# Optimization experiments

Measured on AMD Instinct MI355X. Metric: run time of the kernel, lower is better.

The kernel has to match this reference:

```python
import jax, jax.numpy as jnp
import numpy as np

EPS = 1e-6

def setup_inputs() -> dict:
    key = jax.random.key(0)
    k1, k2, k3 = jax.random.split(key, 3)
    D = 1024
    return {
        "x": jax.random.normal(k1, (2, 2048, D), dtype=jnp.float32),
        "w_norm": jnp.ones((D,), dtype=jnp.float32),
        "w_qkv": jax.random.normal(k2, (3 * D, D), dtype=jnp.float32) * (1.0 / np.sqrt(D)),
        "w_out": jax.random.normal(k3, (D, D), dtype=jnp.float32) * (1.0 / np.sqrt(D)),
        "window_size": 128,
        "n_heads": 16,
    }

def reference(x, w_norm, w_qkv, w_out, window_size, n_heads):
    B, L, D = x.shape
    H = n_heads
    dh = D // H
    skip = x
    # RMSNorm
    rms = jnp.sqrt(jnp.mean(x * x, axis=-1, keepdims=True) + EPS)
    xn = w_norm * (x / rms)
    # QKV projection (torch Linear: y = x @ W.T)
    qkv = xn @ w_qkv.T  # [B, L, 3D]
    q, k, v = jnp.split(qkv, 3, axis=-1)
    q = q.reshape(B, L, H, dh).transpose(0, 2, 1, 3)  # [B,H,L,dh]
    k = k.reshape(B, L, H, dh).transpose(0, 2, 1, 3)
    v = v.reshape(B, L, H, dh).transpose(0, 2, 1, 3)
    scores = jnp.einsum("bhid,bhjd->bhij", q, k) / np.sqrt(dh)  # [B,H,L,L]
    # Symmetric window: token i attends to j in [i - w//2, i + w//2]
    idx = jnp.arange(L)
    half = window_size // 2
    band = jnp.abs(idx[:, None] - idx[None, :]) <= half  # [L, L]
    scores = jnp.where(band, scores, -jnp.inf)
    attn = jax.nn.softmax(scores, axis=-1)  # zeros outside band, matches torch loop
    out = jnp.einsum("bhij,bhjd->bhid", attn, v)  # [B,H,L,dh]
    out = out.transpose(0, 2, 1, 3).reshape(B, L, D)
    out = out @ w_out.T
    return out + skip
```

## Files before the change

### kernel.cpp

```cpp
#include <hip/hip_runtime.h>
#include <hip/hip_bf16.h>
#include <cstdint>

typedef float f32x4 __attribute__((ext_vector_type(4)));
typedef float f32x16 __attribute__((ext_vector_type(16)));
typedef short s16x8 __attribute__((ext_vector_type(8)));
typedef short s16x4 __attribute__((ext_vector_type(4)));
typedef unsigned int u32x2 __attribute__((ext_vector_type(2)));
typedef unsigned int u32x4 __attribute__((ext_vector_type(4)));

constexpr int B_ = 2, L_ = 2048, D_ = 1024, H_ = 16, DH = 64, HALF = 64;
constexpr int M_ROWS = B_ * L_;
constexpr int QKV_N = 3 * D_;

__device__ __forceinline__ void gload16(const void* g, void* l) {
    __builtin_amdgcn_global_load_lds(
        (const __attribute__((address_space(1))) unsigned int*)g,
        (__attribute__((address_space(3))) unsigned int*)l, 16, 0, 0);
}

__device__ __forceinline__ void cfence() {
    __builtin_amdgcn_sched_barrier(0);
    asm volatile("" ::: "memory");
}

__global__ __launch_bounds__(256) void prep_kernel(const float* __restrict__ x,
                                                   const float* __restrict__ wn,
                                                   const float* __restrict__ wq,
                                                   const float* __restrict__ wo,
                                                   __hip_bfloat16* __restrict__ xn,
                                                   __hip_bfloat16* __restrict__ oq,
                                                   __hip_bfloat16* __restrict__ oo) {
    constexpr int NQ4 = QKV_N * D_ / 4;
    constexpr int NCVT = NQ4 + D_ * D_ / 4;
    constexpr int CVTBLK = NCVT / 256;
    int bid = blockIdx.x;
    if (bid < CVTBLK) {
        int i = bid * 256 + threadIdx.x;
        const float* src; __hip_bfloat16* dst; int j;
        if (i < NQ4) { src = wq; dst = oq; j = i; }
        else         { src = wo; dst = oo; j = i - NQ4; }
        float4 v = reinterpret_cast<const float4*>(src)[j];
        s16x4 pk;
        float vals[4] = {v.x, v.y, v.z, v.w};
#pragma unroll
        for (int e = 0; e < 4; ++e) {
            __hip_bfloat16 t = __float2bfloat16(vals[e]);
            pk[e] = *reinterpret_cast<short*>(&t);
        }
        *(s16x4*)(dst + (size_t)j * 4) = pk;
    } else {
        int w = threadIdx.x >> 6, lane = threadIdx.x & 63;
        int row = (bid - CVTBLK) * 4 + w;
        const float4* xr = reinterpret_cast<const float4*>(x + (size_t)row * D_);
        const float4* wr = reinterpret_cast<const float4*>(wn);
        float4 v[4];
        float ss = 0.f;
#pragma unroll
        for (int c = 0; c < 4; ++c) {
            v[c] = xr[c * 64 + lane];
            ss += v[c].x * v[c].x + v[c].y * v[c].y + v[c].z * v[c].z + v[c].w * v[c].w;
        }
#pragma unroll
        for (int off = 32; off; off >>= 1) ss += __shfl_xor(ss, off);
        float rinv = rsqrtf(ss * (1.0f / D_) + 1e-6f);
#pragma unroll
        for (int c = 0; c < 4; ++c) {
            float4 wv = wr[c * 64 + lane];
            s16x4 pk;
            float vals[4] = {v[c].x * rinv * wv.x, v[c].y * rinv * wv.y,
                             v[c].z * rinv * wv.z, v[c].w * rinv * wv.w};
#pragma unroll
            for (int e = 0; e < 4; ++e) {
                __hip_bfloat16 t = __float2bfloat16(vals[e]);
                pk[e] = *reinterpret_cast<short*>(&t);
            }
            *(s16x4*)(xn + (size_t)row * D_ + (c * 64 + lane) * 4) = pk;
        }
    }
}

template <int EPI, int BN>
__global__ __launch_bounds__(256, 2) void gemm_pipe_kernel(const __hip_bfloat16* __restrict__ A,
                                                           const __hip_bfloat16* __restrict__ Bt,
                                                           __hip_bfloat16* __restrict__ Cbf,
                                                           __hip_bfloat16* __restrict__ vT,
                                                           float* __restrict__ Cf,
                                                           const float* __restrict__ resid,
                                                           int M, int N, int K) {
    constexpr int BM = 128;
    constexpr int NFR = BN / 32;
    constexpr int ABYTES = BM * 128;
    constexpr int BBYTES = BN * 128;
    constexpr int BUF = ABYTES + BBYTES;
    constexpr int AISS = BM / 32, BISS = BN / 32, NISS = AISS + BISS;
    __shared__ __align__(16) char smem[2 * BUF];

    const int tid = threadIdx.x;
    const int lane = tid & 63;
    const int wid = tid >> 6;

    int nwg = gridDim.x * gridDim.y;
    int lin = blockIdx.y * gridDim.x + blockIdx.x;
    int cpx = nwg >> 3;
    int swz = (lin & 7) * cpx + (lin >> 3);
    int bx = swz % gridDim.x;
    int by = swz / gridDim.x;

    const int rowBase = by * BM;
    const int colBase = bx * BN;
    const int NTILES = K >> 6;

    const int srow = tid >> 3;
    const int colSw = ((tid & 7) ^ (srow & 7)) << 3;
    const __hip_bfloat16* aG = A + (size_t)(rowBase + srow) * K + colSw;
    const __hip_bfloat16* bG = Bt + (size_t)(colBase + srow) * K + colSw;
    const int dstW = wid << 10;

    const int wm = wid >> 1, wn = wid & 1;
    const int l15 = lane & 15, hi = lane >> 4;
    const int s7 = l15 & 7;
    const int rA = wm * 64 + l15;
    const int rB = wn * (BN / 2) + l15;

    f32x4 acc[4][NFR];
#pragma unroll
    for (int m = 0; m < 4; ++m)
#pragma unroll
        for (int n = 0; n < NFR; ++n) acc[m][n] = (f32x4){0.f, 0.f, 0.f, 0.f};

#pragma unroll
    for (int i = 0; i < AISS; ++i) gload16(aG + (size_t)(i * 32) * K, smem + i * 4096 + dstW);
#pragma unroll
    for (int i = 0; i < BISS; ++i) gload16(bG + (size_t)(i * 32) * K, smem + ABYTES + i * 4096 + dstW);

    for (int kt = 0; kt < NTILES; ++kt) {
        const int bf = kt & 1;
        if (kt + 1 < NTILES) {
            char* base = smem + (bf ^ 1) * BUF;
            const __hip_bfloat16* as = aG + (size_t)(kt + 1) * 64;
            const __hip_bfloat16* bs = bG + (size_t)(kt + 1) * 64;
#pragma unroll
            for (int i = 0; i < AISS; ++i) gload16(as + (size_t)(i * 32) * K, base + i * 4096 + dstW);
#pragma unroll
            for (int i = 0; i < BISS; ++i) gload16(bs + (size_t)(i * 32) * K, base + ABYTES + i * 4096 + dstW);
            if constexpr (NISS == 8)
                asm volatile("s_waitcnt vmcnt(8)" ::: "memory");
            else
                asm volatile("s_waitcnt vmcnt(6)" ::: "memory");
        } else {
            asm volatile("s_waitcnt vmcnt(0)" ::: "memory");
        }
        __builtin_amdgcn_s_barrier();
        cfence();

        const char* ab = smem + bf * BUF;
        const char* bb = ab + ABYTES;
        s16x8 af[4][2], bfr[NFR][2];
#pragma unroll
        for (int mf = 0; mf < 4; ++mf)
#pragma unroll
            for (int kk = 0; kk < 2; ++kk)
                af[mf][kk] = *(const s16x8*)(ab + (rA + mf * 16) * 128 + (((kk * 4 + hi) ^ s7) << 4));
#pragma unroll
        for (int nf = 0; nf < NFR; ++nf)
#pragma unroll
            for (int kk = 0; kk < 2; ++kk)
                bfr[nf][kk] = *(const s16x8*)(bb + (rB + nf * 16) * 128 + (((kk * 4 + hi) ^ s7) << 4));

        __builtin_amdgcn_s_setprio(1);
#pragma unroll
        for (int kk = 0; kk < 2; ++kk)
#pragma unroll
            for (int mf = 0; mf < 4; ++mf)
#pragma unroll
                for (int nf = 0; nf < NFR; ++nf)
                    acc[mf][nf] = __builtin_amdgcn_mfma_f32_16x16x32_bf16(af[mf][kk], bfr[nf][kk],
                                                                          acc[mf][nf], 0, 0, 0);
        __builtin_amdgcn_s_setprio(0);

        asm volatile("s_waitcnt lgkmcnt(0)" ::: "memory");
        __builtin_amdgcn_s_barrier();
        cfence();
    }

    if constexpr (EPI == 0) {
        if (colBase < 2 * D_) {
#pragma unroll
            for (int mf = 0; mf < 4; ++mf)
#pragma unroll
                for (int nf = 0; nf < NFR; ++nf) {
                    int col = colBase + wn * (BN / 2) + nf * 16 + l15;
                    int row0 = rowBase + wm * 64 + mf * 16 + 4 * hi;
#pragma unroll
                    for (int r = 0; r < 4; ++r)
                        Cbf[(size_t)(row0 + r) * N + col] = __float2bfloat16(acc[mf][nf][r]);
                }
        } else {
            char* Ct = smem;
#pragma unroll
            for (int mf = 0; mf < 4; ++mf)
#pragma unroll
                for (int nf = 0; nf < NFR; ++nf) {
                    int cl = wn * (BN / 2) + nf * 16 + l15;
#pragma unroll
                    for (int r = 0; r < 4; ++r) {
                        int rl = wm * 64 + mf * 16 + 4 * hi + r;
                        __hip_bfloat16 t = __float2bfloat16(acc[mf][nf][r]);
                        *(short*)(Ct + cl * 272 + rl * 2) = *reinterpret_cast<short*>(&t);
                    }
                }
            __syncthreads();
            int cl = tid >> 1, half = tid & 1;
            int gcol = colBase + cl - 2 * D_;
            int hh = gcol >> 6, dd = gcol & 63;
            int bb2 = rowBase >> 11, i0 = rowBase & (L_ - 1);
            __hip_bfloat16* dstp = vT + ((size_t)(bb2 * H_ + hh) * DH + dd) * L_ + i0 + half * 64;
#pragma unroll
            for (int ch = 0; ch < 8; ++ch) {
                s16x8 vv = *(const s16x8*)(Ct + cl * 272 + half * 128 + ch * 16);
                *(s16x8*)(dstp + ch * 8) = vv;
            }
        }
    } else {
#pragma unroll
        for (int mf = 0; mf < 4; ++mf)
#pragma unroll
            for (int nf = 0; nf < NFR; ++nf) {
                int col = colBase + wn * (BN / 2) + nf * 16 + l15;
                int row0 = rowBase + wm * 64 + mf * 16 + 4 * hi;
#pragma unroll
                for (int r = 0; r < 4; ++r)
                    Cf[(size_t)(row0 + r) * N + col] = acc[mf][nf][r] + resid[(size_t)(row0 + r) * N + col];
            }
    }
}

__global__ __launch_bounds__(128, 2) void attn_mfma_kernel(const __hip_bfloat16* __restrict__ qkv,
                                                           const __hip_bfloat16* __restrict__ vT,
                                                           __hip_bfloat16* __restrict__ attn) {
    int tid = threadIdx.x;
    int w = tid >> 6;
    int lane = tid & 63;
    int l31 = lane & 31, hi1 = lane >> 5;
    int tq = blockIdx.x, h = blockIdx.y, b = blockIdx.z;
    int qbase = tq * 64 + 32 * w;
    int kb = qbase - HALF;
    int qg = qbase + l31;
    const __hip_bfloat16* qkvb = qkv + (size_t)(b * L_) * QKV_N;
    const __hip_bfloat16* vTg = vT + (size_t)(b * H_ + h) * DH * L_;

    s16x8 qf[4];
#pragma unroll
    for (int kk = 0; kk < 4; ++kk)
        qf[kk] = *(const s16x8*)(qkvb + (size_t)qg * QKV_N + h * DH + kk * 16 + hi1 * 8);

    f32x16 T[5];
#pragma unroll
    for (int kt = 0; kt < 5; ++kt) T[kt] = (f32x16)(0.f);
#pragma unroll
    for (int kt = 0; kt < 5; ++kt) {
        int keyg = kb + 32 * kt + l31;
        int kc = keyg < 0 ? 0 : (keyg > L_ - 1 ? L_ - 1 : keyg);
        const __hip_bfloat16* kp = qkvb + (size_t)kc * QKV_N + D_ + h * DH + hi1 * 8;
#pragma unroll
        for (int kk = 0; kk < 4; ++kk) {
            s16x8 kf = *(const s16x8*)(kp + kk * 16);
            T[kt] = __builtin_amdgcn_mfma_f32_32x32x16_bf16(kf, qf[kk], T[kt], 0, 0, 0);
        }
    }

    float mx = -1e30f;
#pragma unroll
    for (int kt = 0; kt < 5; ++kt) {
#pragma unroll
        for (int r = 0; r < 16; ++r) {
            int koff = (r & 3) + 8 * (r >> 2) + 4 * hi1;
            int keyg = kb + 32 * kt + koff;
            int del = keyg - qg;
            bool ok = (del >= -HALF) && (del <= HALF) && (keyg >= 0) && (keyg < L_);
            float t = ok ? T[kt][r] * 0.125f : -1e30f;
            T[kt][r] = t;
            mx = fmaxf(mx, t);
        }
    }
    mx = fmaxf(mx, __shfl_xor(mx, 32));
    float sum = 0.f;
#pragma unroll
    for (int kt = 0; kt < 5; ++kt) {
#pragma unroll
        for (int r = 0; r < 16; ++r) {
            float p = __expf(T[kt][r] - mx);
            T[kt][r] = p;
            sum += p;
        }
    }
    sum += __shfl_xor(sum, 32);
    float inv = 1.0f / sum;

    u32x4 pu[10];
#pragma unroll
    for (int kt = 0; kt < 5; ++kt) {
#pragma unroll
        for (int s = 0; s < 2; ++s) {
            unsigned P0, P1, P2, P3;
            asm("v_cvt_pk_bf16_f32 %0, %1, %2" : "=v"(P0) : "v"(T[kt][8 * s + 0]), "v"(T[kt][8 * s + 1]));
            asm("v_cvt_pk_bf16_f32 %0, %1, %2" : "=v"(P1) : "v"(T[kt][8 * s + 2]), "v"(T[kt][8 * s + 3]));
            asm("v_cvt_pk_bf16_f32 %0, %1, %2" : "=v"(P2) : "v"(T[kt][8 * s + 4]), "v"(T[kt][8 * s + 5]));
            asm("v_cvt_pk_bf16_f32 %0, %1, %2" : "=v"(P3) : "v"(T[kt][8 * s + 6]), "v"(T[kt][8 * s + 7]));
            u32x2 sA = __builtin_amdgcn_permlane32_swap(P0, P2, false, false);
            u32x2 sB = __builtin_amdgcn_permlane32_swap(P1, P3, false, false);
            pu[2 * kt + s] = (u32x4){sA[0], sB[0], sA[1], sB[1]};
        }
    }

    f32x16 O[2];
#pragma unroll
    for (int dt = 0; dt < 2; ++dt) O[dt] = (f32x16)(0.f);
#pragma unroll
    for (int t = 0; t < 10; ++t) {
        int kv = kb + 16 * t + 8 * hi1;
        kv = kv < 0 ? 0 : (kv > L_ - 8 ? L_ - 8 : kv);
        s16x8 pf = __builtin_bit_cast(s16x8, pu[t]);
#pragma unroll
        for (int dt = 0; dt < 2; ++dt) {
            s16x8 vf = *(const s16x8*)(vTg + (size_t)(32 * dt + l31) * L_ + kv);
            O[dt] = __builtin_amdgcn_mfma_f32_32x32x16_bf16(vf, pf, O[dt], 0, 0, 0);
        }
    }

    __hip_bfloat16* ob = attn + (size_t)(b * L_ + qg) * D_ + h * DH;
#pragma unroll
    for (int dt = 0; dt < 2; ++dt) {
#pragma unroll
        for (int rr = 0; rr < 4; ++rr) {
            s16x4 pk4;
#pragma unroll
            for (int j = 0; j < 4; ++j) {
                __hip_bfloat16 tb = __float2bfloat16(O[dt][4 * rr + j] * inv);
                pk4[j] = *reinterpret_cast<short*>(&tb);
            }
            *(s16x4*)(ob + 32 * dt + 8 * rr + 4 * hi1) = pk4;
        }
    }
}

extern "C" void kernel_launch(void* const* d_in, const int* in_sizes, int n_in,
                              void* d_out, int out_size, void* d_ws, size_t ws_size,
                              hipStream_t stream) {
    const float* x      = (const float*)d_in[0];
    const float* w_norm = (const float*)d_in[1];
    const float* w_qkv  = (const float*)d_in[2];
    const float* w_out  = (const float*)d_in[3];

    char* ws = (char*)d_ws;
    __hip_bfloat16* xn   = (__hip_bfloat16*)(ws);
    __hip_bfloat16* wq   = (__hip_bfloat16*)(ws + (8u  << 20));
    __hip_bfloat16* wo   = (__hip_bfloat16*)(ws + (14u << 20));
    __hip_bfloat16* qkv  = (__hip_bfloat16*)(ws + (16u << 20));
    __hip_bfloat16* attn = (__hip_bfloat16*)(ws + (40u << 20));
    __hip_bfloat16* vT   = (__hip_bfloat16*)(ws + (48u << 20));
    float* out = (float*)d_out;

    prep_kernel<<<4096 + M_ROWS / 4, 256, 0, stream>>>(x, w_norm, w_qkv, w_out, xn, wq, wo);

    gemm_pipe_kernel<0, 128><<<dim3(QKV_N / 128, M_ROWS / 128), 256, 0, stream>>>(
        xn, wq, qkv, vT, nullptr, nullptr, M_ROWS, QKV_N, D_);

    attn_mfma_kernel<<<dim3(L_ / 64, H_, B_), 128, 0, stream>>>(qkv, vT, attn);

    gemm_pipe_kernel<1, 64><<<dim3(D_ / 64, M_ROWS / 128), 256, 0, stream>>>(
        attn, wo, nullptr, nullptr, out, x, M_ROWS, D_, D_);
}
```

Measured before the change: 86.25 us.

## Switch GEMM to four-stage LDS ring with 32-wide K tiles

Replaces the double-buffered 64-wide K-tile loop with a four-slot ring of 32-wide K tiles, prefetching two tiles ahead. It uses a new swizzled LDS layout for loads and reads, and drops one barrier per iteration. The output GEMM gets a higher minimum-waves launch bound. The goal is to hide global-load latency better, at the cost of more loop iterations with fewer MFMAs each and possible register pressure under the tighter launch bound.

```diff
diff --git a/kernel.cpp b/kernel.cpp
--- a/kernel.cpp
+++ b/kernel.cpp
@@ -80,21 +80,21 @@
     }
 }
 
-template <int EPI, int BN>
-__global__ __launch_bounds__(256, 2) void gemm_pipe_kernel(const __hip_bfloat16* __restrict__ A,
-                                                           const __hip_bfloat16* __restrict__ Bt,
-                                                           __hip_bfloat16* __restrict__ Cbf,
-                                                           __hip_bfloat16* __restrict__ vT,
-                                                           float* __restrict__ Cf,
-                                                           const float* __restrict__ resid,
-                                                           int M, int N, int K) {
+template <int EPI, int BN, int MINW>
+__global__ __launch_bounds__(256, MINW) void gemm_pipe_kernel(const __hip_bfloat16* __restrict__ A,
+                                                              const __hip_bfloat16* __restrict__ Bt,
+                                                              __hip_bfloat16* __restrict__ Cbf,
+                                                              __hip_bfloat16* __restrict__ vT,
+                                                              float* __restrict__ Cf,
+                                                              const float* __restrict__ resid,
+                                                              int M, int N, int K) {
     constexpr int BM = 128;
     constexpr int NFR = BN / 32;
-    constexpr int ABYTES = BM * 128;
-    constexpr int BBYTES = BN * 128;
-    constexpr int BUF = ABYTES + BBYTES;
-    constexpr int AISS = BM / 32, BISS = BN / 32, NISS = AISS + BISS;
-    __shared__ __align__(16) char smem[2 * BUF];
+    constexpr int ATILE = BM * 64;
+    constexpr int BTILE = BN * 64;
+    constexpr int BUFB = ATILE + BTILE;
+    constexpr int AISS = BM / 64, BISS = BN / 64;
+    __shared__ __align__(16) char smem[4 * BUFB];
 
     const int tid = threadIdx.x;
     const int lane = tid & 63;
@@ -109,19 +109,20 @@
 
     const int rowBase = by * BM;
     const int colBase = bx * BN;
-    const int NTILES = K >> 6;
-
-    const int srow = tid >> 3;
-    const int colSw = ((tid & 7) ^ (srow & 7)) << 3;
-    const __hip_bfloat16* aG = A + (size_t)(rowBase + srow) * K + colSw;
-    const __hip_bfloat16* bG = Bt + (size_t)(colBase + srow) * K + colSw;
+    const int NTILES = K >> 5;
+
+    const int u = (tid & 7) ^ ((tid >> 3) & 7);
+    const int sRow = 2 * (tid >> 3) + (u >> 2);
+    const int sCol = (u & 3) * 8;
+    const __hip_bfloat16* aG = A + (size_t)(rowBase + sRow) * K + sCol;
+    const __hip_bfloat16* bG = Bt + (size_t)(colBase + sRow) * K + sCol;
     const int dstW = wid << 10;
 
     const int wm = wid >> 1, wn = wid & 1;
     const int l15 = lane & 15, hi = lane >> 4;
-    const int s7 = l15 & 7;
-    const int rA = wm * 64 + l15;
-    const int rB = wn * (BN / 2) + l15;
+    const int sRd = (((l15 & 1) << 2) | hi) ^ ((l15 >> 1) & 7);
+    const int aRd = wm * 4096 + (l15 >> 1) * 128 + sRd * 16;
+    const int bRd = ATILE + wn * (BN * 32) + (l15 >> 1) * 128 + sRd * 16;
 
     f32x4 acc[4][NFR];
 #pragma unroll
@@ -129,59 +130,57 @@
 #pragma unroll
         for (int n = 0; n < NFR; ++n) acc[m][n] = (f32x4){0.f, 0.f, 0.f, 0.f};
 
-#pragma unroll
-    for (int i = 0; i < AISS; ++i) gload16(aG + (size_t)(i * 32) * K, smem + i * 4096 + dstW);
-#pragma unroll
-    for (int i = 0; i < BISS; ++i) gload16(bG + (size_t)(i * 32) * K, smem + ABYTES + i * 4096 + dstW);
-
-    for (int kt = 0; kt < NTILES; ++kt) {
-        const int bf = kt & 1;
-        if (kt + 1 < NTILES) {
-            char* base = smem + (bf ^ 1) * BUF;
-            const __hip_bfloat16* as = aG + (size_t)(kt + 1) * 64;
-            const __hip_bfloat16* bs = bG + (size_t)(kt + 1) * 64;
-#pragma unroll
-            for (int i = 0; i < AISS; ++i) gload16(as + (size_t)(i * 32) * K, base + i * 4096 + dstW);
-#pragma unroll
-            for (int i = 0; i < BISS; ++i) gload16(bs + (size_t)(i * 32) * K, base + ABYTES + i * 4096 + dstW);
-            if constexpr (NISS == 8)
+    auto STAGE = [&](int tt) {
+        char* base = smem + ((tt & 3) * BUFB) + dstW;
+        const __hip_bfloat16* as = aG + (size_t)tt * 32;
+        const __hip_bfloat16* bs = bG + (size_t)tt * 32;
+#pragma unroll
+        for (int j = 0; j < AISS; ++j)
+            gload16(as + (size_t)(j * 64) * K, base + j * 4096);
+#pragma unroll
+        for (int j = 0; j < BISS; ++j)
+            gload16(bs + (size_t)(j * 64) * K, base + ATILE + j * 4096);
+    };
+
+    STAGE(0);
+    STAGE(1);
+
+    for (int t = 0; t < NTILES; ++t) {
+        if (t + 2 < NTILES) {
+            STAGE(t + 2);
+            if constexpr (AISS + BISS == 4)
                 asm volatile("s_waitcnt vmcnt(8)" ::: "memory");
             else
                 asm volatile("s_waitcnt vmcnt(6)" ::: "memory");
+        } else if (t + 1 < NTILES) {
+            if constexpr (AISS + BISS == 4)
+                asm volatile("s_waitcnt vmcnt(4)" ::: "memory");
+            else
+                asm volatile("s_waitcnt vmcnt(3)" ::: "memory");
         } else {
             asm volatile("s_waitcnt vmcnt(0)" ::: "memory");
         }
-        __builtin_amdgcn_s_barrier();
-        cfence();
-
-        const char* ab = smem + bf * BUF;
-        const char* bb = ab + ABYTES;
-        s16x8 af[4][2], bfr[NFR][2];
-#pragma unroll
-        for (int mf = 0; mf < 4; ++mf)
-#pragma unroll
-            for (int kk = 0; kk < 2; ++kk)
-                af[mf][kk] = *(const s16x8*)(ab + (rA + mf * 16) * 128 + (((kk * 4 + hi) ^ s7) << 4));
-#pragma unroll
-        for (int nf = 0; nf < NFR; ++nf)
-#pragma unroll
-            for (int kk = 0; kk < 2; ++kk)
-                bfr[nf][kk] = *(const s16x8*)(bb + (rB + nf * 16) * 128 + (((kk * 4 + hi) ^ s7) << 4));
-
-        __builtin_amdgcn_s_setprio(1);
-#pragma unroll
-        for (int kk = 0; kk < 2; ++kk)
-#pragma unroll
-            for (int mf = 0; mf < 4; ++mf)
-#pragma unroll
-                for (int nf = 0; nf < NFR; ++nf)
-                    acc[mf][nf] = __builtin_amdgcn_mfma_f32_16x16x32_bf16(af[mf][kk], bfr[nf][kk],
-                                                                          acc[mf][nf], 0, 0, 0);
-        __builtin_amdgcn_s_setprio(0);
-
         asm volatile("s_waitcnt lgkmcnt(0)" ::: "memory");
         __builtin_amdgcn_s_barrier();
         cfence();
+
+        const char* tb = smem + ((t & 3) * BUFB);
+        s16x8 af[4], bf[NFR];
+#pragma unroll
+        for (int mf = 0; mf < 4; ++mf)
+            af[mf] = *(const s16x8*)(tb + aRd + mf * 1024);
+#pragma unroll
+        for (int nf = 0; nf < NFR; ++nf)
+            bf[nf] = *(const s16x8*)(tb + bRd + nf * 1024);
+
+        __builtin_amdgcn_s_setprio(1);
+#pragma unroll
+        for (int mf = 0; mf < 4; ++mf)
+#pragma unroll
+            for (int nf = 0; nf < NFR; ++nf)
+                acc[mf][nf] = __builtin_amdgcn_mfma_f32_16x16x32_bf16(af[mf], bf[nf],
+                                                                      acc[mf][nf], 0, 0, 0);
+        __builtin_amdgcn_s_setprio(0);
     }
 
     if constexpr (EPI == 0) {
@@ -364,11 +363,11 @@
 
     prep_kernel<<<4096 + M_ROWS / 4, 256, 0, stream>>>(x, w_norm, w_qkv, w_out, xn, wq, wo);
 
-    gemm_pipe_kernel<0, 128><<<dim3(QKV_N / 128, M_ROWS / 128), 256, 0, stream>>>(
+    gemm_pipe_kernel<0, 128, 2><<<dim3(QKV_N / 128, M_ROWS / 128), 256, 0, stream>>>(
         xn, wq, qkv, vT, nullptr, nullptr, M_ROWS, QKV_N, D_);
 
     attn_mfma_kernel<<<dim3(L_ / 64, H_, B_), 128, 0, stream>>>(qkv, vT, attn);
 
-    gemm_pipe_kernel<1, 64><<<dim3(D_ / 64, M_ROWS / 128), 256, 0, stream>>>(
+    gemm_pipe_kernel<1, 64, 3><<<dim3(D_ / 64, M_ROWS / 128), 256, 0, stream>>>(
         attn, wo, nullptr, nullptr, out, x, M_ROWS, D_, D_);
 }
```

Result: slower. 88.90 us (+3.1%).

## Specialize QKV GEMM with 32-wide K tiles, higher occupancy, vectorized weight conversion

Applied to the files above, without the earlier changes.

Splits the templated GEMM into two dedicated kernels. The QKV GEMM now stages K in 32-wide tiles with a new swizzled LDS layout, halving shared memory so three blocks can be resident per CU, and does a two-pass vectorized V-transpose epilogue. The prep kernel converts 16 floats per thread instead of 4, writing 16-byte stores. The cost is twice as many K iterations with a barrier each, and the smaller tiles may raise sync overhead.

```diff
diff --git a/kernel.cpp b/kernel.cpp
--- a/kernel.cpp
+++ b/kernel.cpp
@@ -31,26 +31,38 @@
                                                    __hip_bfloat16* __restrict__ xn,
                                                    __hip_bfloat16* __restrict__ oq,
                                                    __hip_bfloat16* __restrict__ oo) {
-    constexpr int NQ4 = QKV_N * D_ / 4;
-    constexpr int NCVT = NQ4 + D_ * D_ / 4;
-    constexpr int CVTBLK = NCVT / 256;
+    constexpr int NQ16 = QKV_N * D_ / 16;
+    constexpr int NCVT16 = NQ16 + D_ * D_ / 16;
+    constexpr int CVTBLK = NCVT16 / 256;
     int bid = blockIdx.x;
+    int tid = threadIdx.x;
     if (bid < CVTBLK) {
-        int i = bid * 256 + threadIdx.x;
+        int i = bid * 256 + tid;
         const float* src; __hip_bfloat16* dst; int j;
-        if (i < NQ4) { src = wq; dst = oq; j = i; }
-        else         { src = wo; dst = oo; j = i - NQ4; }
-        float4 v = reinterpret_cast<const float4*>(src)[j];
-        s16x4 pk;
-        float vals[4] = {v.x, v.y, v.z, v.w};
-#pragma unroll
-        for (int e = 0; e < 4; ++e) {
-            __hip_bfloat16 t = __float2bfloat16(vals[e]);
-            pk[e] = *reinterpret_cast<short*>(&t);
-        }
-        *(s16x4*)(dst + (size_t)j * 4) = pk;
+        if (i < NQ16) { src = wq; dst = oq; j = i; }
+        else          { src = wo; dst = oo; j = i - NQ16; }
+        const float4* s4 = reinterpret_cast<const float4*>(src) + (size_t)j * 4;
+        float4 v[4];
+#pragma unroll
+        for (int c = 0; c < 4; ++c) v[c] = s4[c];
+        s16x8 p0, p1;
+#pragma unroll
+        for (int c = 0; c < 2; ++c) {
+            float vals[8] = {v[2*c].x, v[2*c].y, v[2*c].z, v[2*c].w,
+                             v[2*c+1].x, v[2*c+1].y, v[2*c+1].z, v[2*c+1].w};
+            s16x8 pk;
+#pragma unroll
+            for (int e = 0; e < 8; ++e) {
+                __hip_bfloat16 t = __float2bfloat16(vals[e]);
+                pk[e] = *reinterpret_cast<short*>(&t);
+            }
+            if (c == 0) p0 = pk; else p1 = pk;
+        }
+        __hip_bfloat16* o = dst + (size_t)j * 16;
+        *(s16x8*)(o) = p0;
+        *(s16x8*)(o + 8) = p1;
     } else {
-        int w = threadIdx.x >> 6, lane = threadIdx.x & 63;
+        int w = tid >> 6, lane = tid & 63;
         int row = (bid - CVTBLK) * 4 + w;
         const float4* xr = reinterpret_cast<const float4*>(x + (size_t)row * D_);
         const float4* wr = reinterpret_cast<const float4*>(wn);
@@ -80,21 +92,15 @@
     }
 }
 
-template <int EPI, int BN>
-__global__ __launch_bounds__(256, 2) void gemm_pipe_kernel(const __hip_bfloat16* __restrict__ A,
-                                                           const __hip_bfloat16* __restrict__ Bt,
-                                                           __hip_bfloat16* __restrict__ Cbf,
-                                                           __hip_bfloat16* __restrict__ vT,
-                                                           float* __restrict__ Cf,
-                                                           const float* __restrict__ resid,
-                                                           int M, int N, int K) {
-    constexpr int BM = 128;
-    constexpr int NFR = BN / 32;
-    constexpr int ABYTES = BM * 128;
-    constexpr int BBYTES = BN * 128;
-    constexpr int BUF = ABYTES + BBYTES;
-    constexpr int AISS = BM / 32, BISS = BN / 32, NISS = AISS + BISS;
-    __shared__ __align__(16) char smem[2 * BUF];
+__global__ __launch_bounds__(256, 3) void gemm_qkv_kernel(const __hip_bfloat16* __restrict__ A,
+                                                          const __hip_bfloat16* __restrict__ Bt,
+                                                          __hip_bfloat16* __restrict__ Cbf,
+                                                          __hip_bfloat16* __restrict__ vT,
+                                                          int M, int N, int K) {
+    constexpr int BOFF = 8192;
+    constexpr int BUFB = 16384;
+    constexpr int NT = 32;
+    __shared__ __align__(16) char smem[2 * BUFB];
 
     const int tid = threadIdx.x;
     const int lane = tid & 63;
@@ -107,6 +113,146 @@
     int bx = swz % gridDim.x;
     int by = swz / gridDim.x;
 
+    const int rowBase = by * 128;
+    const int colBase = bx * 128;
+
+    const int sR = tid >> 3;
+    const int su = (tid & 7) ^ (sR & 7);
+    const int sMrow = 2 * sR + (su >> 2);
+    const int sCol = (su & 3) * 8;
+    const __hip_bfloat16* aG0 = A + (size_t)(rowBase + sMrow) * K + sCol;
+    const __hip_bfloat16* aG1 = aG0 + (size_t)64 * K;
+    const __hip_bfloat16* bG0 = Bt + (size_t)(colBase + sMrow) * K + sCol;
+    const __hip_bfloat16* bG1 = bG0 + (size_t)64 * K;
+    const int dstW = wid << 10;
+
+    const int wm = wid >> 1, wn = wid & 1;
+    const int l15 = lane & 15, hi = lane >> 4;
+    const int sRd = (((l15 & 1) << 2) | hi) ^ ((l15 >> 1) & 7);
+    const int aRd = wm * 4096 + (l15 >> 1) * 128 + sRd * 16;
+    const int bRd = BOFF + wn * 4096 + (l15 >> 1) * 128 + sRd * 16;
+
+    f32x4 acc[4][4];
+#pragma unroll
+    for (int m = 0; m < 4; ++m)
+#pragma unroll
+        for (int n = 0; n < 4; ++n) acc[m][n] = (f32x4){0.f, 0.f, 0.f, 0.f};
+
+    auto STG = [&](int tt) {
+        char* base = smem + (tt & 1) * BUFB;
+        gload16(aG0 + (size_t)tt * 32, base + dstW);
+        gload16(aG1 + (size_t)tt * 32, base + 4096 + dstW);
+        gload16(bG0 + (size_t)tt * 32, base + BOFF + dstW);
+        gload16(bG1 + (size_t)tt * 32, base + BOFF + 4096 + dstW);
+    };
+
+    STG(0);
+
+    for (int t = 0; t < NT; ++t) {
+        if (t + 1 < NT) {
+            STG(t + 1);
+            asm volatile("s_waitcnt vmcnt(4)" ::: "memory");
+        } else {
+            asm volatile("s_waitcnt vmcnt(0)" ::: "memory");
+        }
+        __builtin_amdgcn_s_barrier();
+        cfence();
+
+        const char* tb = smem + (t & 1) * BUFB;
+        s16x8 af[4], bf[4];
+#pragma unroll
+        for (int mf = 0; mf < 4; ++mf)
+            af[mf] = *(const s16x8*)(tb + aRd + mf * 1024);
+#pragma unroll
+        for (int nf = 0; nf < 4; ++nf)
+            bf[nf] = *(const s16x8*)(tb + bRd + nf * 1024);
+
+        __builtin_amdgcn_s_setprio(1);
+#pragma unroll
+        for (int mf = 0; mf < 4; ++mf)
+#pragma unroll
+            for (int nf = 0; nf < 4; ++nf)
+                acc[mf][nf] = __builtin_amdgcn_mfma_f32_16x16x32_bf16(af[mf], bf[nf],
+                                                                      acc[mf][nf], 0, 0, 0);
+        __builtin_amdgcn_s_setprio(0);
+
+        asm volatile("s_waitcnt lgkmcnt(0)" ::: "memory");
+        __builtin_amdgcn_s_barrier();
+        cfence();
+    }
+
+    if (colBase < 2 * D_) {
+#pragma unroll
+        for (int mf = 0; mf < 4; ++mf)
+#pragma unroll
+            for (int nf = 0; nf < 4; ++nf) {
+                int col = colBase + wn * 64 + nf * 16 + l15;
+                int row0 = rowBase + wm * 64 + mf * 16 + 4 * hi;
+#pragma unroll
+                for (int r = 0; r < 4; ++r)
+                    Cbf[(size_t)(row0 + r) * N + col] = __float2bfloat16(acc[mf][nf][r]);
+            }
+    } else {
+        __syncthreads();
+        int bb2 = rowBase >> 11, i0 = rowBase & (L_ - 1);
+        char* Ct = smem;
+#pragma unroll
+        for (int p = 0; p < 2; ++p) {
+            if (p) __syncthreads();
+            if (wn == p) {
+#pragma unroll
+                for (int mf = 0; mf < 4; ++mf)
+#pragma unroll
+                    for (int nf = 0; nf < 4; ++nf) {
+                        int cl = nf * 16 + l15;
+                        int rlb = wm * 64 + mf * 16 + 4 * hi;
+                        s16x4 pk;
+#pragma unroll
+                        for (int r = 0; r < 4; ++r) {
+                            __hip_bfloat16 t = __float2bfloat16(acc[mf][nf][r]);
+                            pk[r] = *reinterpret_cast<short*>(&t);
+                        }
+                        *(s16x4*)(Ct + cl * 272 + rlb * 2) = pk;
+                    }
+            }
+            __syncthreads();
+            {
+                int c = tid >> 2, qd = tid & 3;
+                int gcol = colBase + p * 64 + c - 2 * D_;
+                int hh = gcol >> 6, dd = gcol & 63;
+                __hip_bfloat16* dstp = vT + ((size_t)(bb2 * H_ + hh) * DH + dd) * L_ + i0;
+#pragma unroll
+                for (int ch = 0; ch < 4; ++ch) {
+                    int rr = qd * 32 + ch * 8;
+                    *(s16x8*)(dstp + rr) = *(const s16x8*)(Ct + c * 272 + rr * 2);
+                }
+            }
+        }
+    }
+}
+
+__global__ __launch_bounds__(256, 2) void gemm_proj_kernel(const __hip_bfloat16* __restrict__ A,
+                                                           const __hip_bfloat16* __restrict__ Bt,
+                                                           float* __restrict__ Cf,
+                                                           const float* __restrict__ resid,
+                                                           int M, int N, int K) {
+    constexpr int BM = 128, BN = 64;
+    constexpr int ABYTES = BM * 128;
+    constexpr int BBYTES = BN * 128;
+    constexpr int BUF = ABYTES + BBYTES;
+    __shared__ __align__(16) char smem[2 * BUF];
+
+    const int tid = threadIdx.x;
+    const int lane = tid & 63;
+    const int wid = tid >> 6;
+
+    int nwg = gridDim.x * gridDim.y;
+    int lin = blockIdx.y * gridDim.x + blockIdx.x;
+    int cpx = nwg >> 3;
+    int swz = (lin & 7) * cpx + (lin >> 3);
+    int bx = swz % gridDim.x;
+    int by = swz / gridDim.x;
+
     const int rowBase = by * BM;
     const int colBase = bx * BN;
     const int NTILES = K >> 6;
@@ -121,49 +267,46 @@
     const int l15 = lane & 15, hi = lane >> 4;
     const int s7 = l15 & 7;
     const int rA = wm * 64 + l15;
-    const int rB = wn * (BN / 2) + l15;
-
-    f32x4 acc[4][NFR];
+    const int rB = wn * 32 + l15;
+
+    f32x4 acc[4][2];
 #pragma unroll
     for (int m = 0; m < 4; ++m)
 #pragma unroll
-        for (int n = 0; n < NFR; ++n) acc[m][n] = (f32x4){0.f, 0.f, 0.f, 0.f};
-
-#pragma unroll
-    for (int i = 0; i < AISS; ++i) gload16(aG + (size_t)(i * 32) * K, smem + i * 4096 + dstW);
-#pragma unroll
-    for (int i = 0; i < BISS; ++i) gload16(bG + (size_t)(i * 32) * K, smem + ABYTES + i * 4096 + dstW);
+        for (int n = 0; n < 2; ++n) acc[m][n] = (f32x4){0.f, 0.f, 0.f, 0.f};
+
+#pragma unroll
+    for (int i = 0; i < 4; ++i) gload16(aG + (size_t)(i * 32) * K, smem + i * 4096 + dstW);
+#pragma unroll
+    for (int i = 0; i < 2; ++i) gload16(bG + (size_t)(i * 32) * K, smem + ABYTES + i * 4096 + dstW);
 
     for (int kt = 0; kt < NTILES; ++kt) {
-        const int bf = kt & 1;
+        const int bf_ = kt & 1;
         if (kt + 1 < NTILES) {
-            char* base = smem + (bf ^ 1) * BUF;
+            char* base = smem + (bf_ ^ 1) * BUF;
             const __hip_bfloat16* as = aG + (size_t)(kt + 1) * 64;
             const __hip_bfloat16* bs = bG + (size_t)(kt + 1) * 64;
 #pragma unroll
-            for (int i = 0; i < AISS; ++i) gload16(as + (size_t)(i * 32) * K, base + i * 4096 + dstW);
-#pragma unroll
-            for (int i = 0; i < BISS; ++i) gload16(bs + (size_t)(i * 32) * K, base + ABYTES + i * 4096 + dstW);
-            if constexpr (NISS == 8)
-                asm volatile("s_waitcnt vmcnt(8)" ::: "memory");
-            else
-                asm volatile("s_waitcnt vmcnt(6)" ::: "memory");
+            for (int i = 0; i < 4; ++i) gload16(as + (size_t)(i * 32) * K, base + i * 4096 + dstW);
+#pragma unroll
+            for (int i = 0; i < 2; ++i) gload16(bs + (size_t)(i * 32) * K, base + ABYTES + i * 4096 + dstW);
+            asm volatile("s_waitcnt vmcnt(6)" ::: "memory");
         } else {
             asm volatile("s_waitcnt vmcnt(0)" ::: "memory");
         }
         __builtin_amdgcn_s_barrier();
         cfence();
 
-        const char* ab = smem + bf * BUF;
+        const char* ab = smem + bf_ * BUF;
         const char* bb = ab + ABYTES;
-        s16x8 af[4][2], bfr[NFR][2];
+        s16x8 af[4][2], bfr[2][2];
 #pragma unroll
         for (int mf = 0; mf < 4; ++mf)
 #pragma unroll
             for (int kk = 0; kk < 2; ++kk)
                 af[mf][kk] = *(const s16x8*)(ab + (rA + mf * 16) * 128 + (((kk * 4 + hi) ^ s7) << 4));
 #pragma unroll
-        for (int nf = 0; nf < NFR; ++nf)
+        for (int nf = 0; nf < 2; ++nf)
 #pragma unroll
             for (int kk = 0; kk < 2; ++kk)
                 bfr[nf][kk] = *(const s16x8*)(bb + (rB + nf * 16) * 128 + (((kk * 4 + hi) ^ s7) << 4));
@@ -174,7 +317,7 @@
 #pragma unroll
             for (int mf = 0; mf < 4; ++mf)
 #pragma unroll
-                for (int nf = 0; nf < NFR; ++nf)
+                for (int nf = 0; nf < 2; ++nf)
                     acc[mf][nf] = __builtin_amdgcn_mfma_f32_16x16x32_bf16(af[mf][kk], bfr[nf][kk],
                                                                           acc[mf][nf], 0, 0, 0);
         __builtin_amdgcn_s_setprio(0);
@@ -184,56 +327,16 @@
         cfence();
     }
 
-    if constexpr (EPI == 0) {
-        if (colBase < 2 * D_) {
-#pragma unroll
-            for (int mf = 0; mf < 4; ++mf)
-#pragma unroll
-                for (int nf = 0; nf < NFR; ++nf) {
-                    int col = colBase + wn * (BN / 2) + nf * 16 + l15;
-                    int row0 = rowBase + wm * 64 + mf * 16 + 4 * hi;
-#pragma unroll
-                    for (int r = 0; r < 4; ++r)
-                        Cbf[(size_t)(row0 + r) * N + col] = __float2bfloat16(acc[mf][nf][r]);
-                }
-        } else {
-            char* Ct = smem;
-#pragma unroll
-            for (int mf = 0; mf < 4; ++mf)
-#pragma unroll
-                for (int nf = 0; nf < NFR; ++nf) {
-                    int cl = wn * (BN / 2) + nf * 16 + l15;
-#pragma unroll
-                    for (int r = 0; r < 4; ++r) {
-                        int rl = wm * 64 + mf * 16 + 4 * hi + r;
-                        __hip_bfloat16 t = __float2bfloat16(acc[mf][nf][r]);
-                        *(short*)(Ct + cl * 272 + rl * 2) = *reinterpret_cast<short*>(&t);
-                    }
-                }
-            __syncthreads();
-            int cl = tid >> 1, half = tid & 1;
-            int gcol = colBase + cl - 2 * D_;
-            int hh = gcol >> 6, dd = gcol & 63;
-            int bb2 = rowBase >> 11, i0 = rowBase & (L_ - 1);
-            __hip_bfloat16* dstp = vT + ((size_t)(bb2 * H_ + hh) * DH + dd) * L_ + i0 + half * 64;
-#pragma unroll
-            for (int ch = 0; ch < 8; ++ch) {
-                s16x8 vv = *(const s16x8*)(Ct + cl * 272 + half * 128 + ch * 16);
-                *(s16x8*)(dstp + ch * 8) = vv;
-            }
-        }
-    } else {
-#pragma unroll
-        for (int mf = 0; mf < 4; ++mf)
-#pragma unroll
-            for (int nf = 0; nf < NFR; ++nf) {
-                int col = colBase + wn * (BN / 2) + nf * 16 + l15;
-                int row0 = rowBase + wm * 64 + mf * 16 + 4 * hi;
-#pragma unroll
-                for (int r = 0; r < 4; ++r)
-                    Cf[(size_t)(row0 + r) * N + col] = acc[mf][nf][r] + resid[(size_t)(row0 + r) * N + col];
-            }
-    }
+#pragma unroll
+    for (int mf = 0; mf < 4; ++mf)
+#pragma unroll
+        for (int nf = 0; nf < 2; ++nf) {
+            int col = colBase + wn * 32 + nf * 16 + l15;
+            int row0 = rowBase + wm * 64 + mf * 16 + 4 * hi;
+#pragma unroll
+            for (int r = 0; r < 4; ++r)
+                Cf[(size_t)(row0 + r) * N + col] = acc[mf][nf][r] + resid[(size_t)(row0 + r) * N + col];
+        }
 }
 
 __global__ __launch_bounds__(128, 2) void attn_mfma_kernel(const __hip_bfloat16* __restrict__ qkv,
@@ -362,13 +465,13 @@
     __hip_bfloat16* vT   = (__hip_bfloat16*)(ws + (48u << 20));
     float* out = (float*)d_out;
 
-    prep_kernel<<<4096 + M_ROWS / 4, 256, 0, stream>>>(x, w_norm, w_qkv, w_out, xn, wq, wo);
-
-    gemm_pipe_kernel<0, 128><<<dim3(QKV_N / 128, M_ROWS / 128), 256, 0, stream>>>(
-        xn, wq, qkv, vT, nullptr, nullptr, M_ROWS, QKV_N, D_);
+    prep_kernel<<<1024 + M_ROWS / 4, 256, 0, stream>>>(x, w_norm, w_qkv, w_out, xn, wq, wo);
+
+    gemm_qkv_kernel<<<dim3(QKV_N / 128, M_ROWS / 128), 256, 0, stream>>>(
+        xn, wq, qkv, vT, M_ROWS, QKV_N, D_);
 
     attn_mfma_kernel<<<dim3(L_ / 64, H_, B_), 128, 0, stream>>>(qkv, vT, attn);
 
-    gemm_pipe_kernel<1, 64><<<dim3(D_ / 64, M_ROWS / 128), 256, 0, stream>>>(
-        attn, wo, nullptr, nullptr, out, x, M_ROWS, D_, D_);
-}
+    gemm_proj_kernel<<<dim3(D_ / 64, M_ROWS / 128), 256, 0, stream>>>(
+        attn, wo, out, x, M_ROWS, D_, D_);
+}
```

Result: no change. 87.96 us (+2.0%).
